# Optimization experiments

Measured on AMD Instinct MI355X. Metric: run time of the kernel, lower is better.

## Reference

```python
import jax, jax.numpy as jnp
import numpy as np

TOP_K = 10
RANKING_WEIGHT = 0.3
UP_WEIGHT = 1.0
DOWN_WEIGHT = 0.5
NEG = 1e9  # finite stand-in for -inf so softmax/grads stay NaN-free


def setup_inputs() -> dict:
    key = jax.random.key(0)
    k1, k2, k3, k4 = jax.random.split(key, 4)
    B, N = 1024, 5000
    up_logits = jax.random.normal(k1, (B, N), jnp.float32)
    down_logits = jax.random.normal(k2, (B, N), jnp.float32)
    y_true = jax.random.normal(k3, (B, N), jnp.float32) * 0.05  # daily returns
    masks = jax.random.randint(k4, (B, N), 0, 2).astype(jnp.int32)
    return {"up_logits": up_logits, "down_logits": down_logits,
            "y_true": y_true, "masks": masks}


def _bce_with_logits(x, z):
    # softplus(x) - x*z  ==  -[z*log(sig(x)) + (1-z)*log(1-sig(x))]
    return jax.nn.softplus(x) - x * z


def reference(up_logits, down_logits, y_true, masks):
    maskb = masks > 0                                   # [B, N]
    maskf = maskb.astype(up_logits.dtype)
    num_valid = maskf.sum(-1)                           # [B]
    nv_safe = jnp.maximum(num_valid, 1.0)
    k = jnp.minimum(TOP_K, num_valid.astype(jnp.int32))  # [B] min(top_k, num)

    # Descending rank of y_true among valid entries (invalid pushed to bottom).
    y_desc = jnp.where(maskb, y_true, -NEG)
    rank_desc = jnp.argsort(jnp.argsort(-y_desc, axis=-1), axis=-1)  # [B, N]
    up_labels = (rank_desc < k[:, None]).astype(up_logits.dtype)

    # Ascending rank (biggest losers) for down path.
    y_asc = jnp.where(maskb, y_true, NEG)
    rank_asc = jnp.argsort(jnp.argsort(y_asc, axis=-1), axis=-1)
    down_labels = (rank_asc < k[:, None]).astype(down_logits.dtype)

    # Mean BCE over valid entries per row.
    up_loss = jnp.sum(_bce_with_logits(up_logits, up_labels) * maskf, -1) / nv_safe
    down_loss = jnp.sum(_bce_with_logits(down_logits, down_labels) * maskf, -1) / nv_safe

    # Listwise KL: softmax over valid entries; kl_div(log p, q, 'batchmean')
    # with 1D input of size num divides the sum by num.
    logp = jax.nn.log_softmax(jnp.where(maskb, up_logits, -NEG), axis=-1)
    logq = jax.nn.log_softmax(jnp.where(maskb, y_true, -NEG), axis=-1)
    q = jnp.exp(logq)
    kl = jnp.sum(jnp.where(maskb, q * (logq - logp), 0.0), -1) / nv_safe

    batch_loss = UP_WEIGHT * up_loss + DOWN_WEIGHT * down_loss + RANKING_WEIGHT * kl
    batch_loss = jnp.where(num_valid > 0, batch_loss, 0.0)  # skip empty rows
    return jnp.sum(batch_loss) / up_logits.shape[0]
```

## Files before the change

kernel.cpp:

```cpp
#include <hip/hip_runtime.h>
#include <math.h>

#define NCOLS 5000
#define NF4   1250
#define QF4   313
#define BLOCK 256
#define NWAVES 4
#define TOPKK 10
#define TR    3
#define CAP   64
#define OUTK  16


__device__ __forceinline__ unsigned mono_f32(float f) {
  unsigned u = __float_as_uint(f);
  return (u & 0x80000000u) ? ~u : (u | 0x80000000u);
}
__device__ __forceinline__ float wave_sum_f(float v) {
#pragma unroll
  for (int o = 1; o < 64; o <<= 1) v += __shfl_xor(v, o);
  return v;
}
__device__ __forceinline__ int wave_sum_i(int v) {
#pragma unroll
  for (int o = 1; o < 64; o <<= 1) v += __shfl_xor(v, o);
  return v;
}
__device__ __forceinline__ unsigned wave_max_u(unsigned v) {
#pragma unroll
  for (int o = 1; o < 64; o <<= 1) {
    unsigned w = __shfl_xor(v, o);
    v = w > v ? w : v;
  }
  return v;
}
__device__ __forceinline__ void gl_lds16(const float4* g, float4* l) {
  __builtin_amdgcn_global_load_lds(
      (const __attribute__((address_space(1))) void*)(g),
      (__attribute__((address_space(3))) void*)(l), 16, 0, 0);
}

extern "C" __global__ __launch_bounds__(BLOCK, 8)
void part_kernel(const float* __restrict__ up, const float* __restrict__ down,
                 const float* __restrict__ yt, const int* __restrict__ masks,
                 float* __restrict__ ws_sums, float2* __restrict__ ws_top,
                 float2* __restrict__ ws_bot) {
  __shared__ float4 y_s[320], u_s[320], d_s[320];
  __shared__ float red_f[7][NWAVES];
  __shared__ unsigned t1w_t[NWAVES], t1w_b[NWAVES];
  __shared__ unsigned keys_t[CAP]; __shared__ int col_t[CAP];
  __shared__ unsigned keys_b[CAP]; __shared__ int col_b[CAP];
  __shared__ int ct, cb;

  const int tid = threadIdx.x;
  const int lane = tid & 63;
  const int wv = tid >> 6;
  const int bq = blockIdx.x;
  const int row = bq >> 2;
  const int q = bq & 3;
  const int qlen = (q == 3) ? (NF4 - 3 * QF4) : QF4;
  const long long b4 = (long long)row * NF4 + q * QF4;

  if (tid == 0) { ct = 0; cb = 0; }

  const float4* yt4q = (const float4*)yt + b4;
  const float4* up4q = (const float4*)up + b4;
  const float4* dn4q = (const float4*)down + b4;
  const int4*   mk4q = (const int4*)masks + b4;

  const int4 mA = mk4q[tid];
  int4 mB = make_int4(0, 0, 0, 0);
  if (wv == 0) mB = mk4q[(256 + tid < qlen) ? (256 + tid) : (qlen - 1)];
  __builtin_amdgcn_sched_barrier(0);

  {
    const int wb = wv * 64;
    gl_lds16(yt4q + wb + lane, y_s + wb);
    gl_lds16(up4q + wb + lane, u_s + wb);
    gl_lds16(dn4q + wb + lane, d_s + wb);
    if (wv == 0) {
      const int fB = (256 + lane < qlen) ? (256 + lane) : (qlen - 1);
      gl_lds16(yt4q + fB, y_s + 256);
      gl_lds16(up4q + fB, u_s + 256);
      gl_lds16(dn4q + fB, d_s + 256);
    }
  }
  __builtin_amdgcn_sched_barrier(0);

  int vmask = 0;
  float sq = 0.f, sp = 0.f, seyy = 0.f, seyu = 0.f;
  float pu = 1.f, pd = 1.f;
  unsigned tmax = 0u, tbmax = 0u;

#define ELEM(bit, Y, U, D, M, INB)                                      \
  {                                                                     \
    const bool valid = (INB) && ((M) > 0);                              \
    const float y = (Y), u = (U), d = (D);                              \
    const unsigned kd = valid ? mono_f32(y) : 0u;                       \
    const unsigned kb2 = valid ? ~kd : 0u;                              \
    vmask |= valid ? (1 << (bit)) : 0;                                  \
    tmax = kd > tmax ? kd : tmax;                                       \
    tbmax = kb2 > tbmax ? kb2 : tbmax;                                  \
    const float mf = valid ? 1.f : 0.f;                                 \
    const float ey = __expf(y);                                         \
    const float eu = __expf(u);                                         \
    const float ed = __expf(d);                                         \
    const float mey = mf * ey;                                          \
    sq += mey;                                                          \
    seyy = fmaf(mey, y, seyy);                                          \
    seyu = fmaf(mey, u, seyu);                                          \
    sp += mf * eu;                                                      \
    pu *= valid ? (1.f + eu) : 1.f;                                     \
    pd *= valid ? (1.f + ed) : 1.f;                                     \
  }

#define CHUNKA()                                                        \
  {                                                                     \
    const float4 yv = y_s[tid];                                         \
    const float4 uv = u_s[tid];                                         \
    const float4 dv = d_s[tid];                                         \
    ELEM(0, yv.x, uv.x, dv.x, mA.x, true)                               \
    ELEM(1, yv.y, uv.y, dv.y, mA.y, true)                               \
    ELEM(2, yv.z, uv.z, dv.z, mA.z, true)                               \
    ELEM(3, yv.w, uv.w, dv.w, mA.w, true)                               \
  }
#define CHUNKB()                                                        \
  {                                                                     \
    const bool inbB = (256 + tid) < qlen;                               \
    const float4 yv = y_s[256 + tid];                                   \
    const float4 uv = u_s[256 + tid];                                   \
    const float4 dv = d_s[256 + tid];                                   \
    ELEM(4, yv.x, uv.x, dv.x, mB.x, inbB)                               \
    ELEM(5, yv.y, uv.y, dv.y, mB.y, inbB)                               \
    ELEM(6, yv.z, uv.z, dv.z, mB.z, inbB)                               \
    ELEM(7, yv.w, uv.w, dv.w, mB.w, inbB)                               \
  }

  if (wv == 0) {
    asm volatile("s_waitcnt vmcnt(3)" ::: "memory");
    __builtin_amdgcn_sched_barrier(0);
    CHUNKA()
    asm volatile("s_waitcnt vmcnt(0)" ::: "memory");
    __builtin_amdgcn_sched_barrier(0);
    CHUNKB()
  } else {
    asm volatile("s_waitcnt vmcnt(0)" ::: "memory");
    __builtin_amdgcn_sched_barrier(0);
    CHUNKA()
  }
#undef CHUNKA
#undef CHUNKB
#undef ELEM

  const float aspu = __logf(pu);
  const float aspd = __logf(pd);

  int nv_l = wave_sum_i(__popc((unsigned)vmask));
  sq = wave_sum_f(sq);
  sp = wave_sum_f(sp);
  seyy = wave_sum_f(seyy);
  seyu = wave_sum_f(seyu);
  const float au = wave_sum_f(aspu);
  const float ad = wave_sum_f(aspd);

  unsigned t1t = 0u, t1b_ = 0u;
  {
    unsigned vt = tmax, vb = tbmax;
#pragma unroll
    for (int r = 0; r < TR; ++r) {
      const unsigned mt = wave_max_u(vt);
      const unsigned mb_ = wave_max_u(vb);
      if (vt == mt) vt = 0u;
      if (vb == mb_) vb = 0u;
      t1t = mt; t1b_ = mb_;
    }
  }
  if (lane == 0) {
    red_f[0][wv] = (float)nv_l;
    red_f[1][wv] = sq;  red_f[2][wv] = sp;
    red_f[3][wv] = seyy; red_f[4][wv] = seyu;
    red_f[5][wv] = au;  red_f[6][wv] = ad;
    t1w_t[wv] = t1t; t1w_b[wv] = t1b_;
  }
  __syncthreads();

  unsigned t1 = t1w_t[0], t1b = t1w_b[0];
#pragma unroll
  for (int w = 1; w < NWAVES; ++w) {
    t1 = t1w_t[w] < t1 ? t1w_t[w] : t1;
    t1b = t1w_b[w] < t1b ? t1w_b[w] : t1b;
  }
  const int nv_q = (int)(red_f[0][0] + red_f[0][1] + red_f[0][2] + red_f[0][3]);

  {
    const int mbA = vmask & 0xF;
    if (mbA) {
      const float4 yv = y_s[tid];
      const float ya[4] = {yv.x, yv.y, yv.z, yv.w};
#pragma unroll
      for (int c = 0; c < 4; ++c) {
        if ((mbA >> c) & 1) {
          const unsigned kd = mono_f32(ya[c]);
          if (kd >= t1) {
            const int i = atomicAdd(&ct, 1);
            if (i < CAP) { keys_t[i] = kd; col_t[i] = (tid << 2) + c; }
          }
          const unsigned kb2 = ~kd;
          if (kb2 >= t1b) {
            const int i = atomicAdd(&cb, 1);
            if (i < CAP) { keys_b[i] = kb2; col_b[i] = (tid << 2) + c; }
          }
        }
      }
    }
    const int mbB = (vmask >> 4) & 0xF;
    if (mbB) {
      const float4 yv = y_s[256 + tid];
      const float ya[4] = {yv.x, yv.y, yv.z, yv.w};
#pragma unroll
      for (int c = 0; c < 4; ++c) {
        if ((mbB >> c) & 1) {
          const unsigned kd = mono_f32(ya[c]);
          if (kd >= t1) {
            const int i = atomicAdd(&ct, 1);
            if (i < CAP) { keys_t[i] = kd; col_t[i] = ((256 + tid) << 2) + c; }
          }
          const unsigned kb2 = ~kd;
          if (kb2 >= t1b) {
            const int i = atomicAdd(&cb, 1);
            if (i < CAP) { keys_b[i] = kb2; col_b[i] = ((256 + tid) << 2) + c; }
          }
        }
      }
    }
  }
  __syncthreads();

  const int kq = nv_q < TOPKK ? nv_q : TOPKK;
  if (wv == 0) {
    const int n = ct < CAP ? ct : CAP;
    const unsigned kc = (lane < n) ? keys_t[lane] : 0u;
    unsigned thr = 0u;
#pragma unroll
    for (int bb = 31; bb >= 0; --bb) {
      const unsigned t = thr | (1u << bb);
      thr = (__popcll(__ballot(kc >= t)) >= kq) ? t : thr;
    }
    const bool sel = (kc >= thr) && (kc != 0u);
    const unsigned long long msk = __ballot(sel);
    const int idx = __popcll(msk & ((1ull << lane) - 1ull));
    if (sel && idx < OUTK)
      ws_top[bq * OUTK + idx] =
          make_float2(__uint_as_float(kc), ((const float*)u_s)[col_t[lane]]);
    int cnt = __popcll(msk);
    cnt = cnt < OUTK ? cnt : OUTK;
    if (lane >= cnt && lane < OUTK)
      ws_top[bq * OUTK + lane] = make_float2(0.f, 0.f);
  } else if (wv == 1) {
    const int n = cb < CAP ? cb : CAP;
    const unsigned kc = (lane < n) ? keys_b[lane] : 0u;
    unsigned thr = 0u;
#pragma unroll
    for (int bb = 31; bb >= 0; --bb) {
      const unsigned t = thr | (1u << bb);
      thr = (__popcll(__ballot(kc >= t)) >= kq) ? t : thr;
    }
    const bool sel = (kc >= thr) && (kc != 0u);
    const unsigned long long msk = __ballot(sel);
    const int idx = __popcll(msk & ((1ull << lane) - 1ull));
    if (sel && idx < OUTK)
      ws_bot[bq * OUTK + idx] =
          make_float2(__uint_as_float(kc), ((const float*)d_s)[col_b[lane]]);
    int cnt = __popcll(msk);
    cnt = cnt < OUTK ? cnt : OUTK;
    if (lane >= cnt && lane < OUTK)
      ws_bot[bq * OUTK + lane] = make_float2(0.f, 0.f);
  } else if (wv == 2 && lane < 8) {
    const float s = (lane < 7)
        ? red_f[lane][0] + red_f[lane][1] + red_f[lane][2] + red_f[lane][3]
        : 0.f;
    ws_sums[bq * 8 + lane] = s;
  }
}

extern "C" __global__ __launch_bounds__(256, 8)
void finish_kernel(const float* __restrict__ ws_sums,
                   const float2* __restrict__ ws_top,
                   const float2* __restrict__ ws_bot,
                   float* __restrict__ out, int nrows, float inv_nrows) {
  __shared__ float wl[NWAVES];
  const int tid = threadIdx.x;
  const int lane = tid & 63;
  const int wv = tid >> 6;
  const int row = blockIdx.x * NWAVES + wv;

  float loss = 0.f;
  if (row < nrows) {
    float v = 0.f;
    if (lane < 32) v = ws_sums[(row * 4 + (lane >> 3)) * 8 + (lane & 7)];
    v += __shfl_xor(v, 8);
    v += __shfl_xor(v, 16);
    const float nvf = __shfl(v, 0);
    const int nv = (int)nvf;
    if (nv > 0) {
      const int k = nv < TOPKK ? nv : TOPKK;
      const float2 a = ws_top[row * 64 + lane];
      const float2 bt = ws_bot[row * 64 + lane];
      const unsigned kt = __float_as_uint(a.x);
      const unsigned kb = __float_as_uint(bt.x);
      unsigned thr_t = 0u, thr_b = 0u;
#pragma unroll
      for (int bb = 31; bb >= 0; --bb) {
        const unsigned tt = thr_t | (1u << bb);
        const unsigned tb = thr_b | (1u << bb);
        thr_t = (__popcll(__ballot(kt >= tt)) >= k) ? tt : thr_t;
        thr_b = (__popcll(__ballot(kb >= tb)) >= k) ? tb : thr_b;
      }
      const float su = wave_sum_f((kt >= thr_t && kt != 0u) ? a.y : 0.f);
      const float sd = wave_sum_f((kb >= thr_b && kb != 0u) ? bt.y : 0.f);
      const float SQ = __shfl(v, 1), SP = __shfl(v, 2);
      const float SYY = __shfl(v, 3), SYU = __shfl(v, 4);
      const float ASU = __shfl(v, 5), ASD = __shfl(v, 6);
      const float kl = (SYY - SYU) / SQ - __logf(SQ) + __logf(SP);
      loss = ((ASU - su) + 0.5f * (ASD - sd) + 0.3f * kl) / nvf;
    }
  }
  if (lane == 0) wl[wv] = loss;
  __syncthreads();
  if (tid == 0)
    atomicAdd(out, (wl[0] + wl[1] + wl[2] + wl[3]) * inv_nrows);
}

extern "C" void kernel_launch(void* const* d_in, const int* in_sizes, int n_in,
                              void* d_out, int out_size, void* d_ws, size_t ws_size,
                              hipStream_t stream) {
  const float* up_logits   = (const float*)d_in[0];
  const float* down_logits = (const float*)d_in[1];
  const float* y_true      = (const float*)d_in[2];
  const int*   masks       = (const int*)d_in[3];

  const int nrows = in_sizes[0] / NCOLS;
  const int nrq = nrows * 4;

  float* wsf = (float*)d_ws;
  float* ws_sums = wsf;
  float2* ws_top = (float2*)(wsf + (size_t)nrq * 8);
  float2* ws_bot = ws_top + (size_t)nrq * OUTK;
  (void)ws_size;

  hipMemsetAsync(d_out, 0, sizeof(float) * (size_t)out_size, stream);
  part_kernel<<<nrq, BLOCK, 0, stream>>>(up_logits, down_logits, y_true, masks,
                                         ws_sums, ws_top, ws_bot);
  finish_kernel<<<(nrows + NWAVES - 1) / NWAVES, 256, 0, stream>>>(
      ws_sums, ws_top, ws_bot, (float*)d_out, nrows, 1.0f / (float)nrows);
}
```

Measured before the change: 122.4 us.

## Split rows into five 250-float4 slices with direct register loads, dropping LDS staging

Each row is now split across five blocks of 250 float4s instead of four blocks of ~313, so every thread handles exactly one float4 and the ragged second chunk handled by wave 0 goes away. Inputs are loaded straight into registers instead of being staged through global-to-LDS loads. Candidate values are kept in shared arrays directly rather than looked up later by column index. The finish kernel merges five partial sums and 50 candidates per row, in exchange for more blocks and more workspace traffic, and with 6 of 256 threads idle per block.

```diff
diff --git a/kernel.cpp b/kernel.cpp
--- a/kernel.cpp
+++ b/kernel.cpp
@@ -3,13 +3,14 @@
 
 #define NCOLS 5000
 #define NF4   1250
-#define QF4   313
+#define FIF   250
+#define NFIF  5
 #define BLOCK 256
 #define NWAVES 4
 #define TOPKK 10
 #define TR    3
 #define CAP   64
-#define OUTK  16
+#define OUTK  10
 
 
 __device__ __forceinline__ unsigned mono_f32(float f) {
@@ -33,11 +34,6 @@
     v = w > v ? w : v;
   }
   return v;
-}
-__device__ __forceinline__ void gl_lds16(const float4* g, float4* l) {
-  __builtin_amdgcn_global_load_lds(
-      (const __attribute__((address_space(1))) void*)(g),
-      (__attribute__((address_space(3))) void*)(l), 16, 0, 0);
 }
 
 extern "C" __global__ __launch_bounds__(BLOCK, 8)
@@ -45,60 +41,41 @@
                  const float* __restrict__ yt, const int* __restrict__ masks,
                  float* __restrict__ ws_sums, float2* __restrict__ ws_top,
                  float2* __restrict__ ws_bot) {
-  __shared__ float4 y_s[320], u_s[320], d_s[320];
   __shared__ float red_f[7][NWAVES];
   __shared__ unsigned t1w_t[NWAVES], t1w_b[NWAVES];
-  __shared__ unsigned keys_t[CAP]; __shared__ int col_t[CAP];
-  __shared__ unsigned keys_b[CAP]; __shared__ int col_b[CAP];
+  __shared__ unsigned keys_t[CAP]; __shared__ float vals_t[CAP];
+  __shared__ unsigned keys_b[CAP]; __shared__ float vals_b[CAP];
   __shared__ int ct, cb;
 
   const int tid = threadIdx.x;
   const int lane = tid & 63;
   const int wv = tid >> 6;
   const int bq = blockIdx.x;
-  const int row = bq >> 2;
-  const int q = bq & 3;
-  const int qlen = (q == 3) ? (NF4 - 3 * QF4) : QF4;
-  const long long b4 = (long long)row * NF4 + q * QF4;
+  const long long b4 = (long long)bq * FIF;
 
   if (tid == 0) { ct = 0; cb = 0; }
 
-  const float4* yt4q = (const float4*)yt + b4;
-  const float4* up4q = (const float4*)up + b4;
-  const float4* dn4q = (const float4*)down + b4;
-  const int4*   mk4q = (const int4*)masks + b4;
-
-  const int4 mA = mk4q[tid];
-  int4 mB = make_int4(0, 0, 0, 0);
-  if (wv == 0) mB = mk4q[(256 + tid < qlen) ? (256 + tid) : (qlen - 1)];
-  __builtin_amdgcn_sched_barrier(0);
-
-  {
-    const int wb = wv * 64;
-    gl_lds16(yt4q + wb + lane, y_s + wb);
-    gl_lds16(up4q + wb + lane, u_s + wb);
-    gl_lds16(dn4q + wb + lane, d_s + wb);
-    if (wv == 0) {
-      const int fB = (256 + lane < qlen) ? (256 + lane) : (qlen - 1);
-      gl_lds16(yt4q + fB, y_s + 256);
-      gl_lds16(up4q + fB, u_s + 256);
-      gl_lds16(dn4q + fB, d_s + 256);
-    }
-  }
-  __builtin_amdgcn_sched_barrier(0);
-
-  int vmask = 0;
+  const bool inb = tid < FIF;
+  const int fc = inb ? tid : FIF - 1;
+
+  const float4 y4 = ((const float4*)yt)[b4 + fc];
+  const float4 u4 = ((const float4*)up)[b4 + fc];
+  const float4 d4 = ((const float4*)down)[b4 + fc];
+  const int4   m4 = ((const int4*)masks)[b4 + fc];
+
+  int nv_l = 0;
   float sq = 0.f, sp = 0.f, seyy = 0.f, seyu = 0.f;
   float pu = 1.f, pd = 1.f;
   unsigned tmax = 0u, tbmax = 0u;
-
-#define ELEM(bit, Y, U, D, M, INB)                                      \
+  unsigned kk[4]; float ua[4], da[4];
+
+#define ELEM(c, Y, U, D, M)                                             \
   {                                                                     \
-    const bool valid = (INB) && ((M) > 0);                              \
+    const bool valid = inb && ((M) > 0);                                \
     const float y = (Y), u = (U), d = (D);                              \
     const unsigned kd = valid ? mono_f32(y) : 0u;                       \
     const unsigned kb2 = valid ? ~kd : 0u;                              \
-    vmask |= valid ? (1 << (bit)) : 0;                                  \
+    kk[c] = kd; ua[c] = u; da[c] = d;                                   \
     tmax = kd > tmax ? kd : tmax;                                       \
     tbmax = kb2 > tbmax ? kb2 : tbmax;                                  \
     const float mf = valid ? 1.f : 0.f;                                 \
@@ -106,6 +83,7 @@
     const float eu = __expf(u);                                         \
     const float ed = __expf(d);                                         \
     const float mey = mf * ey;                                          \
+    nv_l += valid ? 1 : 0;                                              \
     sq += mey;                                                          \
     seyy = fmaf(mey, y, seyy);                                          \
     seyu = fmaf(mey, u, seyu);                                          \
@@ -114,48 +92,16 @@
     pd *= valid ? (1.f + ed) : 1.f;                                     \
   }
 
-#define CHUNKA()                                                        \
-  {                                                                     \
-    const float4 yv = y_s[tid];                                         \
-    const float4 uv = u_s[tid];                                         \
-    const float4 dv = d_s[tid];                                         \
-    ELEM(0, yv.x, uv.x, dv.x, mA.x, true)                               \
-    ELEM(1, yv.y, uv.y, dv.y, mA.y, true)                               \
-    ELEM(2, yv.z, uv.z, dv.z, mA.z, true)                               \
-    ELEM(3, yv.w, uv.w, dv.w, mA.w, true)                               \
-  }
-#define CHUNKB()                                                        \
-  {                                                                     \
-    const bool inbB = (256 + tid) < qlen;                               \
-    const float4 yv = y_s[256 + tid];                                   \
-    const float4 uv = u_s[256 + tid];                                   \
-    const float4 dv = d_s[256 + tid];                                   \
-    ELEM(4, yv.x, uv.x, dv.x, mB.x, inbB)                               \
-    ELEM(5, yv.y, uv.y, dv.y, mB.y, inbB)                               \
-    ELEM(6, yv.z, uv.z, dv.z, mB.z, inbB)                               \
-    ELEM(7, yv.w, uv.w, dv.w, mB.w, inbB)                               \
-  }
-
-  if (wv == 0) {
-    asm volatile("s_waitcnt vmcnt(3)" ::: "memory");
-    __builtin_amdgcn_sched_barrier(0);
-    CHUNKA()
-    asm volatile("s_waitcnt vmcnt(0)" ::: "memory");
-    __builtin_amdgcn_sched_barrier(0);
-    CHUNKB()
-  } else {
-    asm volatile("s_waitcnt vmcnt(0)" ::: "memory");
-    __builtin_amdgcn_sched_barrier(0);
-    CHUNKA()
-  }
-#undef CHUNKA
-#undef CHUNKB
+  ELEM(0, y4.x, u4.x, d4.x, m4.x)
+  ELEM(1, y4.y, u4.y, d4.y, m4.y)
+  ELEM(2, y4.z, u4.z, d4.z, m4.z)
+  ELEM(3, y4.w, u4.w, d4.w, m4.w)
 #undef ELEM
 
   const float aspu = __logf(pu);
   const float aspd = __logf(pd);
 
-  int nv_l = wave_sum_i(__popc((unsigned)vmask));
+  nv_l = wave_sum_i(nv_l);
   sq = wave_sum_f(sq);
   sp = wave_sum_f(sp);
   seyy = wave_sum_f(seyy);
@@ -192,45 +138,18 @@
   }
   const int nv_q = (int)(red_f[0][0] + red_f[0][1] + red_f[0][2] + red_f[0][3]);
 
-  {
-    const int mbA = vmask & 0xF;
-    if (mbA) {
-      const float4 yv = y_s[tid];
-      const float ya[4] = {yv.x, yv.y, yv.z, yv.w};
-#pragma unroll
-      for (int c = 0; c < 4; ++c) {
-        if ((mbA >> c) & 1) {
-          const unsigned kd = mono_f32(ya[c]);
-          if (kd >= t1) {
-            const int i = atomicAdd(&ct, 1);
-            if (i < CAP) { keys_t[i] = kd; col_t[i] = (tid << 2) + c; }
-          }
-          const unsigned kb2 = ~kd;
-          if (kb2 >= t1b) {
-            const int i = atomicAdd(&cb, 1);
-            if (i < CAP) { keys_b[i] = kb2; col_b[i] = (tid << 2) + c; }
-          }
-        }
+#pragma unroll
+  for (int c = 0; c < 4; ++c) {
+    const unsigned kd = kk[c];
+    if (kd != 0u) {
+      if (kd >= t1) {
+        const int i = atomicAdd(&ct, 1);
+        if (i < CAP) { keys_t[i] = kd; vals_t[i] = ua[c]; }
       }
-    }
-    const int mbB = (vmask >> 4) & 0xF;
-    if (mbB) {
-      const float4 yv = y_s[256 + tid];
-      const float ya[4] = {yv.x, yv.y, yv.z, yv.w};
-#pragma unroll
-      for (int c = 0; c < 4; ++c) {
-        if ((mbB >> c) & 1) {
-          const unsigned kd = mono_f32(ya[c]);
-          if (kd >= t1) {
-            const int i = atomicAdd(&ct, 1);
-            if (i < CAP) { keys_t[i] = kd; col_t[i] = ((256 + tid) << 2) + c; }
-          }
-          const unsigned kb2 = ~kd;
-          if (kb2 >= t1b) {
-            const int i = atomicAdd(&cb, 1);
-            if (i < CAP) { keys_b[i] = kb2; col_b[i] = ((256 + tid) << 2) + c; }
-          }
-        }
+      const unsigned kb2 = ~kd;
+      if (kb2 >= t1b) {
+        const int i = atomicAdd(&cb, 1);
+        if (i < CAP) { keys_b[i] = kb2; vals_b[i] = da[c]; }
       }
     }
   }
@@ -250,8 +169,7 @@
     const unsigned long long msk = __ballot(sel);
     const int idx = __popcll(msk & ((1ull << lane) - 1ull));
     if (sel && idx < OUTK)
-      ws_top[bq * OUTK + idx] =
-          make_float2(__uint_as_float(kc), ((const float*)u_s)[col_t[lane]]);
+      ws_top[bq * OUTK + idx] = make_float2(__uint_as_float(kc), vals_t[lane]);
     int cnt = __popcll(msk);
     cnt = cnt < OUTK ? cnt : OUTK;
     if (lane >= cnt && lane < OUTK)
@@ -269,8 +187,7 @@
     const unsigned long long msk = __ballot(sel);
     const int idx = __popcll(msk & ((1ull << lane) - 1ull));
     if (sel && idx < OUTK)
-      ws_bot[bq * OUTK + idx] =
-          make_float2(__uint_as_float(kc), ((const float*)d_s)[col_b[lane]]);
+      ws_bot[bq * OUTK + idx] = make_float2(__uint_as_float(kc), vals_b[lane]);
     int cnt = __popcll(msk);
     cnt = cnt < OUTK ? cnt : OUTK;
     if (lane >= cnt && lane < OUTK)
@@ -296,18 +213,20 @@
 
   float loss = 0.f;
   if (row < nrows) {
-    float v = 0.f;
-    if (lane < 32) v = ws_sums[(row * 4 + (lane >> 3)) * 8 + (lane & 7)];
-    v += __shfl_xor(v, 8);
-    v += __shfl_xor(v, 16);
-    const float nvf = __shfl(v, 0);
+    const float v = (lane < 40) ? ws_sums[row * 40 + lane] : 0.f;
+    float s = v;
+    s += __shfl(v, (lane + 8) & 63);
+    s += __shfl(v, (lane + 16) & 63);
+    s += __shfl(v, (lane + 24) & 63);
+    s += __shfl(v, (lane + 32) & 63);
+    const float nvf = __shfl(s, 0);
     const int nv = (int)nvf;
     if (nv > 0) {
       const int k = nv < TOPKK ? nv : TOPKK;
-      const float2 a = ws_top[row * 64 + lane];
-      const float2 bt = ws_bot[row * 64 + lane];
+      const float2 a  = (lane < 50) ? ws_top[row * 50 + lane] : make_float2(0.f, 0.f);
+      const float2 b2 = (lane < 50) ? ws_bot[row * 50 + lane] : make_float2(0.f, 0.f);
       const unsigned kt = __float_as_uint(a.x);
-      const unsigned kb = __float_as_uint(bt.x);
+      const unsigned kb = __float_as_uint(b2.x);
       unsigned thr_t = 0u, thr_b = 0u;
 #pragma unroll
       for (int bb = 31; bb >= 0; --bb) {
@@ -317,10 +236,10 @@
         thr_b = (__popcll(__ballot(kb >= tb)) >= k) ? tb : thr_b;
       }
       const float su = wave_sum_f((kt >= thr_t && kt != 0u) ? a.y : 0.f);
-      const float sd = wave_sum_f((kb >= thr_b && kb != 0u) ? bt.y : 0.f);
-      const float SQ = __shfl(v, 1), SP = __shfl(v, 2);
-      const float SYY = __shfl(v, 3), SYU = __shfl(v, 4);
-      const float ASU = __shfl(v, 5), ASD = __shfl(v, 6);
+      const float sd = wave_sum_f((kb >= thr_b && kb != 0u) ? b2.y : 0.f);
+      const float SQ = __shfl(s, 1), SP = __shfl(s, 2);
+      const float SYY = __shfl(s, 3), SYU = __shfl(s, 4);
+      const float ASU = __shfl(s, 5), ASD = __shfl(s, 6);
       const float kl = (SYY - SYU) / SQ - __logf(SQ) + __logf(SP);
       loss = ((ASU - su) + 0.5f * (ASD - sd) + 0.3f * kl) / nvf;
     }
@@ -340,16 +259,16 @@
   const int*   masks       = (const int*)d_in[3];
 
   const int nrows = in_sizes[0] / NCOLS;
-  const int nrq = nrows * 4;
+  const int nrf = nrows * NFIF;
 
   float* wsf = (float*)d_ws;
   float* ws_sums = wsf;
-  float2* ws_top = (float2*)(wsf + (size_t)nrq * 8);
-  float2* ws_bot = ws_top + (size_t)nrq * OUTK;
+  float2* ws_top = (float2*)(wsf + (size_t)nrf * 8);
+  float2* ws_bot = ws_top + (size_t)nrf * OUTK;
   (void)ws_size;
 
   hipMemsetAsync(d_out, 0, sizeof(float) * (size_t)out_size, stream);
-  part_kernel<<<nrq, BLOCK, 0, stream>>>(up_logits, down_logits, y_true, masks,
+  part_kernel<<<nrf, BLOCK, 0, stream>>>(up_logits, down_logits, y_true, masks,
                                          ws_sums, ws_top, ws_bot);
   finish_kernel<<<(nrows + NWAVES - 1) / NWAVES, 256, 0, stream>>>(
       ws_sums, ws_top, ws_bot, (float*)d_out, nrows, 1.0f / (float)nrows);
```

After: 125.7 us. 1.03x slower.
